# Kernel tuning notes

Hardware: AMD Instinct MI355X
Metric: run time of the kernel (lower is better)

Reference implementation:

```python
import jax, jax.numpy as jnp
import numpy as np

B, L, D, DFF, DLLM, E, TOPK = 16, 512, 768, 3072, 4096, 8, 2
EPS_GATE = 1e-9
LN_EPS = 1e-5


def _layernorm(x, gamma, beta):
    mu = jnp.mean(x, axis=-1, keepdims=True)
    var = jnp.var(x, axis=-1, keepdims=True)
    return (x - mu) * jax.lax.rsqrt(var + LN_EPS) * gamma + beta


def _mlp_block(x, w1, b1, w2, b2, gamma, beta):
    # MLPBlock: Linear -> GELU -> Linear -> LayerNorm(residual). Dropout is identity in eval.
    h = jax.nn.gelu(x @ w1 + b1)
    o = h @ w2 + b2
    return _layernorm(o + x, gamma, beta)


def setup_inputs() -> dict:
    key = jax.random.key(0)
    ks = jax.random.split(key, 24)
    sd = lambda fan_in: 1.0 / np.sqrt(fan_in)
    inp = {
        'cycle_curve_data': jax.random.normal(ks[0], (B, L, D), jnp.float32),
        'cycle_numbers': jax.random.uniform(ks[1], (B, 1), jnp.float32) * 1000.0,
        'DKP_embeddings': jax.random.normal(ks[2], (B, DLLM), jnp.float32),
        # Gate (PatternRouter_two): fuses LLM embedding + cycle number -> expert logits
        'gate_We': jax.random.normal(ks[3], (DLLM, DFF), jnp.float32) * sd(DLLM),
        'gate_Wc': jax.random.normal(ks[4], (1, DFF), jnp.float32),
        'gate_b': jnp.zeros((DFF,), jnp.float32),
        'gate_Wo': jax.random.normal(ks[5], (DFF, E), jnp.float32) * sd(DFF),
        'gate_bo': jnp.zeros((E,), jnp.float32),
        # Stacked expert params [E, ...]
        'e_w1': jax.random.normal(ks[6], (E, D, DFF), jnp.float32) * sd(D),
        'e_b1': jnp.zeros((E, DFF), jnp.float32),
        'e_w2': jax.random.normal(ks[7], (E, DFF, D), jnp.float32) * sd(DFF),
        'e_b2': jnp.zeros((E, D), jnp.float32),
        'e_gamma': jnp.ones((E, D), jnp.float32),
        'e_beta': jnp.zeros((E, D), jnp.float32),
        # General expert
        'g_w1': jax.random.normal(ks[8], (D, DFF), jnp.float32) * sd(D),
        'g_b1': jnp.zeros((DFF,), jnp.float32),
        'g_w2': jax.random.normal(ks[9], (DFF, D), jnp.float32) * sd(DFF),
        'g_b2': jnp.zeros((D,), jnp.float32),
        'g_gamma': jnp.ones((D,), jnp.float32),
        'g_beta': jnp.zeros((D,), jnp.float32),
    }
    return inp


def reference(cycle_curve_data, cycle_numbers, DKP_embeddings,
              gate_We, gate_Wc, gate_b, gate_Wo, gate_bo,
              e_w1, e_b1, e_w2, e_b2, e_gamma, e_beta,
              g_w1, g_b1, g_w2, g_b2, g_gamma, g_beta):
    # --- Router: clean logits (eval mode: no noise) ---
    h = jax.nn.relu(DKP_embeddings @ gate_We + cycle_numbers @ gate_Wc + gate_b)
    logits = h @ gate_Wo + gate_bo                         # [B, E]
    _, idx = jax.lax.top_k(logits, TOPK)                   # [B, TOPK]
    probs = jax.nn.softmax(logits, axis=1)
    mask = jnp.zeros_like(probs).at[jnp.arange(B)[:, None], idx].set(1.0)
    gated = probs * mask
    gated = gated / (jnp.sum(gated, axis=1, keepdims=True) + EPS_GATE)  # [B, E]

    # --- Experts: dense compute, zero gates zero out non-routed experts ---
    x = cycle_curve_data
    combined = jnp.zeros_like(x)
    for e in range(E):  # small fixed expert count
        out_e = _mlp_block(x, e_w1[e], e_b1[e], e_w2[e], e_b2[e], e_gamma[e], e_beta[e])
        combined = combined + gated[:, e, None, None] * out_e

    general = _mlp_block(x, g_w1, g_b1, g_w2, g_b2, g_gamma, g_beta)
    final_out = general + combined.astype(jnp.bfloat16)  # matches .to(torch.bfloat16) cast before add
    return final_out
```

## Files before the change

kernel.cpp:

```cpp
#include <hip/hip_runtime.h>
#include <cstdint>

#define B_    16
#define L_    512
#define D_    768
#define DFF_  3072
#define DLLM_ 4096
#define E_    8

typedef unsigned short ushort_t;
typedef __attribute__((ext_vector_type(4))) float accfrag_t;
typedef __attribute__((ext_vector_type(8))) short bfrag_t;

typedef __attribute__((address_space(3))) uint32_t lds_u32;
typedef __attribute__((address_space(1))) uint32_t glb_u32;

__device__ inline void gload16(const void* g, void* l) {
  __builtin_amdgcn_global_load_lds((const glb_u32*)(uintptr_t)g,
                                   (lds_u32*)(uint32_t)(uintptr_t)l, 16, 0, 0);
}

__device__ inline ushort_t f2bf(float f) {
  uint32_t u = __float_as_uint(f);
  return (ushort_t)((u + 0x7FFFu + ((u >> 16) & 1u)) >> 16);
}
__device__ inline float bf2f(ushort_t v) { return __uint_as_float(((uint32_t)v) << 16); }

#define MFMA16(a, b, c) __builtin_amdgcn_mfma_f32_16x16x32_bf16(a, b, c, 0, 0, 0)

template <int KT>
__device__ __forceinline__ void gemm_body(const char* gA, const char* gB,
                                          char* sm, accfrag_t acc[4][4]) {
  const int tid = threadIdx.x;
  const int lane = tid & 63;
  const int w = tid >> 6, wm = w >> 1, wn = w & 1;
  const int LDB = KT * 128;

  const int R0 = tid >> 3;
  const char* srcA = gA + (size_t)R0 * LDB + ((((tid & 7) ^ (R0 & 7)) << 4));
  const char* srcB = gB + (size_t)R0 * LDB + ((((tid & 7) ^ (R0 & 7)) << 4));
  const int dl = tid * 16;

  const int l15 = lane & 15, l7 = lane & 7, lhi = lane >> 4;
  const int a0 = (wm * 64 + l15) * 128 + ((lhi ^ l7) << 4);
  const int a1 = (wm * 64 + l15) * 128 + (((4 + lhi) ^ l7) << 4);
  const int b0 = 16384 + (wn * 64 + l15) * 128 + ((lhi ^ l7) << 4);
  const int b1 = 16384 + (wn * 64 + l15) * 128 + (((4 + lhi) ^ l7) << 4);

#pragma unroll 1
  for (int t = 0; t < KT; ++t) {
    const size_t ko = (size_t)t * 128;
#pragma unroll
    for (int j = 0; j < 4; ++j)
      gload16(srcA + (size_t)j * 32 * LDB + ko, sm + j * 4096 + dl);
#pragma unroll
    for (int j = 0; j < 4; ++j)
      gload16(srcB + (size_t)j * 32 * LDB + ko, sm + 16384 + j * 4096 + dl);
    __syncthreads();
    {
      bfrag_t af[4], bf[4];
#pragma unroll
      for (int nf = 0; nf < 4; ++nf) bf[nf] = *(const bfrag_t*)(sm + b0 + nf * 2048);
#pragma unroll
      for (int mf = 0; mf < 4; ++mf) af[mf] = *(const bfrag_t*)(sm + a0 + mf * 2048);
      __builtin_amdgcn_s_setprio(1);
#pragma unroll
      for (int mf = 0; mf < 4; ++mf)
#pragma unroll
        for (int nf = 0; nf < 4; ++nf)
          acc[mf][nf] = MFMA16(af[mf], bf[nf], acc[mf][nf]);
      __builtin_amdgcn_s_setprio(0);
    }
    __builtin_amdgcn_sched_barrier(0);
    {
      bfrag_t af[4], bf[4];
#pragma unroll
      for (int nf = 0; nf < 4; ++nf) bf[nf] = *(const bfrag_t*)(sm + b1 + nf * 2048);
#pragma unroll
      for (int mf = 0; mf < 4; ++mf) af[mf] = *(const bfrag_t*)(sm + a1 + mf * 2048);
      __builtin_amdgcn_s_setprio(1);
#pragma unroll
      for (int mf = 0; mf < 4; ++mf)
#pragma unroll
        for (int nf = 0; nf < 4; ++nf)
          acc[mf][nf] = MFMA16(af[mf], bf[nf], acc[mf][nf]);
      __builtin_amdgcn_s_setprio(0);
    }
    __syncthreads();
  }
}

__device__ inline void job_tile(int f, int tilesPerJob, int jp_count,
                                int& jobIdx, int& t) {
  if ((jp_count & 7) == 0) {
    const int xcd = f & 7, slot = f >> 3;
    jobIdx = xcd + 8 * (slot / tilesPerJob);
    t = slot % tilesPerJob;
  } else {
    jobIdx = f / tilesPerJob;
    t = f % tilesPerJob;
  }
}

__global__ __launch_bounds__(256, 4)
void gemm1_k(const ushort_t* __restrict__ xb, const ushort_t* __restrict__ w1t,
             const float* __restrict__ e_b1, const float* __restrict__ g_b1,
             const int* __restrict__ tidx, ushort_t* __restrict__ h_out,
             int job0, int jp_count) {
  __shared__ char sm[32768];
  int jp, t;
  job_tile(blockIdx.x, 96, jp_count, jp, t);
  const int mt = t / 24, nt = t % 24;
  const int job = job0 + jp;
  const int b = job / 3, s = job - b * 3;
  const int e = (s < 2) ? tidx[b * 2 + s] : E_;
  const char* gA = (const char*)(xb + ((size_t)b * L_ + mt * 128) * D_);
  const char* gB = (const char*)(w1t + ((size_t)e * DFF_ + nt * 128) * D_);
  accfrag_t acc[4][4] = {};
  gemm_body<12>(gA, gB, sm, acc);

  const float* b1 = (s < 2) ? (e_b1 + (size_t)e * DFF_) : g_b1;
  const int lane = threadIdx.x & 63, w = threadIdx.x >> 6;
  const int wm = w >> 1, wn = w & 1;
  const int row0 = mt * 128 + wm * 64 + ((lane >> 4) << 2);
  const int col0 = nt * 128 + wn * 64 + (lane & 15);
  float bias[4];
#pragma unroll
  for (int nf = 0; nf < 4; ++nf) bias[nf] = b1[col0 + nf * 16];
  ushort_t* hp = h_out + (size_t)jp * L_ * DFF_ + (size_t)row0 * DFF_ + col0;
#pragma unroll
  for (int mf = 0; mf < 4; ++mf)
#pragma unroll
    for (int r = 0; r < 4; ++r) {
      ushort_t* hr_ = hp + (size_t)(mf * 16 + r) * DFF_;
#pragma unroll
      for (int nf = 0; nf < 4; ++nf) {
        float v = acc[mf][nf][r] + bias[nf];
        float u = 0.7978845608028654f * (v + 0.044715f * v * v * v);
        float th = 1.0f - 2.0f / (1.0f + __expf(2.0f * u));
        hr_[nf * 16] = f2bf(0.5f * v * (1.0f + th));
      }
    }
}

__global__ __launch_bounds__(256, 4)
void gemm2_k(const ushort_t* __restrict__ h_in, const ushort_t* __restrict__ w2t,
             const float* __restrict__ e_b2, const float* __restrict__ g_b2,
             const float* __restrict__ x_f, const int* __restrict__ tidx,
             ushort_t* __restrict__ slot_o, float* __restrict__ outp,
             int job0, int jp_count) {
  __shared__ char sm[32768];
  int jp, t;
  job_tile(blockIdx.x, 24, jp_count, jp, t);
  const int mt = t / 6, nt = t % 6;
  const int job = job0 + jp;
  const int b = job / 3, s = job - b * 3;
  const int e = (s < 2) ? tidx[b * 2 + s] : E_;
  const char* gA = (const char*)(h_in + ((size_t)jp * L_ + mt * 128) * DFF_);
  const char* gB = (const char*)(w2t + ((size_t)e * D_ + nt * 128) * DFF_);
  accfrag_t acc[4][4] = {};
  gemm_body<48>(gA, gB, sm, acc);

  const float* b2 = (s < 2) ? (e_b2 + (size_t)e * D_) : g_b2;
  const int lane = threadIdx.x & 63, w = threadIdx.x >> 6;
  const int wm = w >> 1, wn = w & 1;
  const int row0 = mt * 128 + wm * 64 + ((lane >> 4) << 2);
  const int col0 = nt * 128 + wn * 64 + (lane & 15);
  float bias[4];
#pragma unroll
  for (int nf = 0; nf < 4; ++nf) bias[nf] = b2[col0 + nf * 16];
#pragma unroll
  for (int mf = 0; mf < 4; ++mf)
#pragma unroll
    for (int r = 0; r < 4; ++r) {
      const int row = row0 + mf * 16 + r;
      const float* xr = x_f + ((size_t)b * L_ + row) * D_ + col0;
#pragma unroll
      for (int nf = 0; nf < 4; ++nf) {
        float v = acc[mf][nf][r] + bias[nf] + xr[nf * 16];
        if (s < 2)
          slot_o[(((size_t)b * 2 + s) * L_ + row) * D_ + col0 + nf * 16] = f2bf(v);
        else
          outp[((size_t)b * L_ + row) * D_ + col0 + nf * 16] = v;
      }
    }
}

__global__ __launch_bounds__(256)
void transpose_cvt_k(const float* __restrict__ srcE, const float* __restrict__ srcG,
                     ushort_t* __restrict__ dst, int R, int C) {
  const int z = blockIdx.z;
  const float* src = (z < 8) ? (srcE + (size_t)z * R * C) : srcG;
  ushort_t* out = dst + (size_t)z * R * C;
  __shared__ float tile[64][65];
  const int c0 = blockIdx.x * 64, r0 = blockIdx.y * 64;
  const int t = threadIdx.x;
  const int rr = t >> 4, cc = (t & 15) * 4;
#pragma unroll
  for (int i = 0; i < 4; ++i) {
    const float4 v = *(const float4*)(src + (size_t)(r0 + rr + i * 16) * C + c0 + cc);
    tile[rr + i * 16][cc] = v.x; tile[rr + i * 16][cc + 1] = v.y;
    tile[rr + i * 16][cc + 2] = v.z; tile[rr + i * 16][cc + 3] = v.w;
  }
  __syncthreads();
  const int c = t >> 2, r8 = (t & 3) * 16;
#pragma unroll
  for (int j = 0; j < 2; ++j) {
    ushort_t u[8];
#pragma unroll
    for (int k = 0; k < 8; ++k) u[k] = f2bf(tile[r8 + j * 8 + k][c]);
    *(uint4*)(out + (size_t)(c0 + c) * R + r0 + r8 + j * 8) = *(const uint4*)u;
  }
}

__global__ void cvt_x_k(const float* __restrict__ in, ushort_t* __restrict__ out) {
  const int i = (blockIdx.x * 256 + threadIdx.x) * 4;
  const float4 v = *(const float4*)(in + i);
  uint2 u;
  u.x = (uint32_t)f2bf(v.x) | ((uint32_t)f2bf(v.y) << 16);
  u.y = (uint32_t)f2bf(v.z) | ((uint32_t)f2bf(v.w) << 16);
  *(uint2*)(out + i) = u;
}

__global__ __launch_bounds__(256)
void router_partial_k(const float* __restrict__ emb, const float* __restrict__ We,
                      float* __restrict__ rp) {
  const int nt = blockIdx.x, kb = blockIdx.y;
  const int tid = threadIdx.x;
  __shared__ float semb[B_][256];
  const int k0 = kb * 256;
#pragma unroll
  for (int r = 0; r < B_; ++r) semb[r][tid] = emb[(size_t)r * DLLM_ + k0 + tid];
  __syncthreads();
  const int f = nt * 256 + tid;
  float acc[B_] = {};
  for (int k = 0; k < 256; ++k) {
    const float wv = We[(size_t)(k0 + k) * DFF_ + f];
#pragma unroll
    for (int j = 0; j < B_; ++j) acc[j] += semb[j][k] * wv;
  }
#pragma unroll
  for (int j = 0; j < B_; ++j)
    rp[((size_t)kb * B_ + j) * DFF_ + f] = acc[j];
}

__global__ void router_reduce_k(const float* __restrict__ rp, const float* __restrict__ cyc,
                                const float* __restrict__ Wc, const float* __restrict__ gb,
                                float* __restrict__ hr) {
  const int g = blockIdx.x * 256 + threadIdx.x;
  const int b = g / DFF_, f = g - b * DFF_;
  float s = 0.0f;
#pragma unroll
  for (int kb = 0; kb < 16; ++kb)
    s += rp[((size_t)kb * B_ + b) * DFF_ + f];
  s += cyc[b] * Wc[f] + gb[f];
  hr[(size_t)b * DFF_ + f] = fmaxf(s, 0.0f);
}

__global__ void router_final_k(const float* __restrict__ hr, const float* __restrict__ Wo,
                               const float* __restrict__ bo, int* __restrict__ tidx,
                               float* __restrict__ gates) {
  const int b = blockIdx.x, tid = threadIdx.x;
  float acc[E_] = {};
  for (int f = tid; f < DFF_; f += 256) {
    const float hv = hr[(size_t)b * DFF_ + f];
#pragma unroll
    for (int o = 0; o < E_; ++o) acc[o] += hv * Wo[(size_t)f * E_ + o];
  }
  __shared__ float lred[E_][4];
#pragma unroll
  for (int o = 0; o < E_; ++o) {
    float v = acc[o];
#pragma unroll
    for (int off = 32; off > 0; off >>= 1) v += __shfl_down(v, off, 64);
    if ((tid & 63) == 0) lred[o][tid >> 6] = v;
  }
  __syncthreads();
  if (tid == 0) {
    float lg[E_];
    float mx = -1e30f;
    for (int o = 0; o < E_; ++o) {
      lg[o] = lred[o][0] + lred[o][1] + lred[o][2] + lred[o][3] + bo[o];
      mx = fmaxf(mx, lg[o]);
    }
    int i1 = 0;
    for (int o = 1; o < E_; ++o) if (lg[o] > lg[i1]) i1 = o;
    int i2 = (i1 == 0) ? 1 : 0;
    for (int o = 0; o < E_; ++o) if (o != i1 && lg[o] > lg[i2]) i2 = o;
    float p[E_], sum = 0.0f;
    for (int o = 0; o < E_; ++o) { p[o] = __expf(lg[o] - mx); sum += p[o]; }
    const float p1 = p[i1] / sum, p2 = p[i2] / sum;
    const float den = p1 + p2 + 1e-9f;
    tidx[b * 2] = i1; tidx[b * 2 + 1] = i2;
    gates[b * 2] = p1 / den; gates[b * 2 + 1] = p2 / den;
  }
}

__global__ __launch_bounds__(256)
void final_ln_k(float* __restrict__ outp, const ushort_t* __restrict__ so,
                const float* __restrict__ gates, const int* __restrict__ tidx,
                const float* __restrict__ e_gam, const float* __restrict__ e_bet,
                const float* __restrict__ g_gam, const float* __restrict__ g_bet) {
  const int row = blockIdx.x;
  const int b = row >> 9, l = row & 511;
  const int tid = threadIdx.x;
  __shared__ float red4[4];
  float* gr = outp + (size_t)row * D_;
  const ushort_t* s0 = so + (((size_t)b * 2 + 0) * L_ + l) * D_;
  const ushort_t* s1 = so + (((size_t)b * 2 + 1) * L_ + l) * D_;
  float a0[3], a1[3], a2[3];
#pragma unroll
  for (int j = 0; j < 3; ++j) {
    const int d = tid + j * 256;
    a0[j] = gr[d];
    a1[j] = bf2f(s0[d]);
    a2[j] = bf2f(s1[d]);
  }
  auto bsum = [&](float v) -> float {
#pragma unroll
    for (int o = 32; o > 0; o >>= 1) v += __shfl_down(v, o, 64);
    if ((tid & 63) == 0) red4[tid >> 6] = v;
    __syncthreads();
    const float r = red4[0] + red4[1] + red4[2] + red4[3];
    __syncthreads();
    return r;
  };
  const float sg = bsum(a0[0] + a0[1] + a0[2]);
  const float qg = bsum(a0[0] * a0[0] + a0[1] * a0[1] + a0[2] * a0[2]);
  const float s0s = bsum(a1[0] + a1[1] + a1[2]);
  const float q0s = bsum(a1[0] * a1[0] + a1[1] * a1[1] + a1[2] * a1[2]);
  const float s1s = bsum(a2[0] + a2[1] + a2[2]);
  const float q1s = bsum(a2[0] * a2[0] + a2[1] * a2[1] + a2[2] * a2[2]);
  const float inv = 1.0f / 768.0f;
  const float mug = sg * inv, rg = rsqrtf(qg * inv - mug * mug + 1e-5f);
  const float mu0 = s0s * inv, r0 = rsqrtf(q0s * inv - mu0 * mu0 + 1e-5f);
  const float mu1 = s1s * inv, r1 = rsqrtf(q1s * inv - mu1 * mu1 + 1e-5f);
  const int e0 = tidx[b * 2], e1 = tidx[b * 2 + 1];
  const float g0 = gates[b * 2], g1 = gates[b * 2 + 1];
#pragma unroll
  for (int j = 0; j < 3; ++j) {
    const int d = tid + j * 256;
    const float lng = (a0[j] - mug) * rg * g_gam[d] + g_bet[d];
    const float ln0 = (a1[j] - mu0) * r0 * e_gam[(size_t)e0 * D_ + d] + e_bet[(size_t)e0 * D_ + d];
    const float ln1 = (a2[j] - mu1) * r1 * e_gam[(size_t)e1 * D_ + d] + e_bet[(size_t)e1 * D_ + d];
    const float comb = g0 * ln0 + g1 * ln1;
    gr[d] = lng + bf2f(f2bf(comb));
  }
}

extern "C" void kernel_launch(void* const* d_in, const int* in_sizes, int n_in,
                              void* d_out, int out_size, void* d_ws, size_t ws_size,
                              hipStream_t stream) {
  const float* x_f  = (const float*)d_in[0];
  const float* cyc  = (const float*)d_in[1];
  const float* emb  = (const float*)d_in[2];
  const float* We   = (const float*)d_in[3];
  const float* Wc   = (const float*)d_in[4];
  const float* gb   = (const float*)d_in[5];
  const float* Wo   = (const float*)d_in[6];
  const float* bo   = (const float*)d_in[7];
  const float* e_w1 = (const float*)d_in[8];
  const float* e_b1 = (const float*)d_in[9];
  const float* e_w2 = (const float*)d_in[10];
  const float* e_b2 = (const float*)d_in[11];
  const float* e_gam = (const float*)d_in[12];
  const float* e_bet = (const float*)d_in[13];
  const float* g_w1 = (const float*)d_in[14];
  const float* g_b1 = (const float*)d_in[15];
  const float* g_w2 = (const float*)d_in[16];
  const float* g_b2 = (const float*)d_in[17];
  const float* g_gam = (const float*)d_in[18];
  const float* g_bet = (const float*)d_in[19];
  float* outp = (float*)d_out;
  char* ws = (char*)d_ws;

  size_t off = 0;
  auto alloc = [&](size_t bytes) { size_t o = off; off = (off + bytes + 255) & ~(size_t)255; return o; };
  const size_t o_idx  = alloc(32 * 4);
  const size_t o_gate = alloc(32 * 4);
  const size_t o_hr   = alloc((size_t)B_ * DFF_ * 4);
  const size_t o_rp   = alloc((size_t)16 * B_ * DFF_ * 4);
  const size_t o_xb   = alloc((size_t)B_ * L_ * D_ * 2);
  const size_t o_w1t  = alloc((size_t)9 * DFF_ * D_ * 2);
  const size_t o_w2t  = alloc((size_t)9 * D_ * DFF_ * 2);
  const size_t o_so   = alloc((size_t)B_ * 2 * L_ * D_ * 2);
  const size_t o_h    = off;

  int JP = 1;
  const int divs[10] = {48, 24, 16, 12, 8, 6, 4, 3, 2, 1};
  for (int k = 0; k < 10; ++k) {
    if (o_h + (size_t)divs[k] * L_ * DFF_ * 2 <= ws_size) { JP = divs[k]; break; }
  }

  ushort_t* xb    = (ushort_t*)(ws + o_xb);
  ushort_t* w1t   = (ushort_t*)(ws + o_w1t);
  ushort_t* w2t   = (ushort_t*)(ws + o_w2t);
  ushort_t* so    = (ushort_t*)(ws + o_so);
  ushort_t* h_ws  = (ushort_t*)(ws + o_h);
  int*      tidx  = (int*)(ws + o_idx);
  float*    gates = (float*)(ws + o_gate);
  float*    hr    = (float*)(ws + o_hr);
  float*    rp    = (float*)(ws + o_rp);

  cvt_x_k<<<dim3((B_ * L_ * D_) / 1024), dim3(256), 0, stream>>>(x_f, xb);
  transpose_cvt_k<<<dim3(DFF_ / 64, D_ / 64, 9), dim3(256), 0, stream>>>(e_w1, g_w1, w1t, D_, DFF_);
  transpose_cvt_k<<<dim3(D_ / 64, DFF_ / 64, 9), dim3(256), 0, stream>>>(e_w2, g_w2, w2t, DFF_, D_);
  router_partial_k<<<dim3(12, 16), dim3(256), 0, stream>>>(emb, We, rp);
  router_reduce_k<<<dim3(192), dim3(256), 0, stream>>>(rp, cyc, Wc, gb, hr);
  router_final_k<<<dim3(16), dim3(256), 0, stream>>>(hr, Wo, bo, tidx, gates);

  const int passes = 48 / JP;
  for (int p = 0; p < passes; ++p) {
    gemm1_k<<<dim3(96 * JP), dim3(256), 0, stream>>>(xb, w1t, e_b1, g_b1, tidx, h_ws, p * JP, JP);
    gemm2_k<<<dim3(24 * JP), dim3(256), 0, stream>>>(h_ws, w2t, e_b2, g_b2, x_f, tidx, so, outp, p * JP, JP);
  }
  final_ln_k<<<dim3(B_ * L_), dim3(256), 0, stream>>>(outp, so, gates, tidx,
                                                      e_gam, e_bet, g_gam, g_bet);
}
```

Baseline: 477.8 us.

## Widen GEMM tiles to 128x192 and fuse router reduce into final router kernel

Both expert GEMMs now use 128x192 output tiles, so each wave holds a 4x6 grid of MFMA accumulators. LDS grows to 40KB and launch bounds drop to 3 blocks per CU. The wider tile raises arithmetic intensity per shared-memory load, at the cost of more registers, lower occupancy and fewer blocks per pass. Separately, the router reduce kernel is folded into router_final_k, which removes one launch and the intermediate hr buffer, though the reduction now runs on only 16 blocks.

Result: faster. 437.3 us (median of 2 runs) (-8.5%).

```diff
diff --git a/kernel.cpp b/kernel.cpp
--- a/kernel.cpp
+++ b/kernel.cpp
@@ -30,22 +30,23 @@
 
 template <int KT>
 __device__ __forceinline__ void gemm_body(const char* gA, const char* gB,
-                                          char* sm, accfrag_t acc[4][4]) {
+                                          char* sm, accfrag_t acc[4][6]) {
   const int tid = threadIdx.x;
   const int lane = tid & 63;
   const int w = tid >> 6, wm = w >> 1, wn = w & 1;
   const int LDB = KT * 128;
 
   const int R0 = tid >> 3;
-  const char* srcA = gA + (size_t)R0 * LDB + ((((tid & 7) ^ (R0 & 7)) << 4));
-  const char* srcB = gB + (size_t)R0 * LDB + ((((tid & 7) ^ (R0 & 7)) << 4));
+  const int swz = (((tid & 7) ^ (R0 & 7)) << 4);
+  const char* srcA = gA + (size_t)R0 * LDB + swz;
+  const char* srcB = gB + (size_t)R0 * LDB + swz;
   const int dl = tid * 16;
 
   const int l15 = lane & 15, l7 = lane & 7, lhi = lane >> 4;
   const int a0 = (wm * 64 + l15) * 128 + ((lhi ^ l7) << 4);
   const int a1 = (wm * 64 + l15) * 128 + (((4 + lhi) ^ l7) << 4);
-  const int b0 = 16384 + (wn * 64 + l15) * 128 + ((lhi ^ l7) << 4);
-  const int b1 = 16384 + (wn * 64 + l15) * 128 + (((4 + lhi) ^ l7) << 4);
+  const int b0 = 16384 + (wn * 96 + l15) * 128 + ((lhi ^ l7) << 4);
+  const int b1 = 16384 + (wn * 96 + l15) * 128 + (((4 + lhi) ^ l7) << 4);
 
 #pragma unroll 1
   for (int t = 0; t < KT; ++t) {
@@ -54,35 +55,35 @@
     for (int j = 0; j < 4; ++j)
       gload16(srcA + (size_t)j * 32 * LDB + ko, sm + j * 4096 + dl);
 #pragma unroll
-    for (int j = 0; j < 4; ++j)
+    for (int j = 0; j < 6; ++j)
       gload16(srcB + (size_t)j * 32 * LDB + ko, sm + 16384 + j * 4096 + dl);
     __syncthreads();
     {
-      bfrag_t af[4], bf[4];
-#pragma unroll
-      for (int nf = 0; nf < 4; ++nf) bf[nf] = *(const bfrag_t*)(sm + b0 + nf * 2048);
+      bfrag_t af[4], bf[6];
+#pragma unroll
+      for (int nf = 0; nf < 6; ++nf) bf[nf] = *(const bfrag_t*)(sm + b0 + nf * 2048);
 #pragma unroll
       for (int mf = 0; mf < 4; ++mf) af[mf] = *(const bfrag_t*)(sm + a0 + mf * 2048);
       __builtin_amdgcn_s_setprio(1);
 #pragma unroll
       for (int mf = 0; mf < 4; ++mf)
 #pragma unroll
-        for (int nf = 0; nf < 4; ++nf)
+        for (int nf = 0; nf < 6; ++nf)
           acc[mf][nf] = MFMA16(af[mf], bf[nf], acc[mf][nf]);
       __builtin_amdgcn_s_setprio(0);
     }
     __builtin_amdgcn_sched_barrier(0);
     {
-      bfrag_t af[4], bf[4];
-#pragma unroll
-      for (int nf = 0; nf < 4; ++nf) bf[nf] = *(const bfrag_t*)(sm + b1 + nf * 2048);
+      bfrag_t af[4], bf[6];
+#pragma unroll
+      for (int nf = 0; nf < 6; ++nf) bf[nf] = *(const bfrag_t*)(sm + b1 + nf * 2048);
 #pragma unroll
       for (int mf = 0; mf < 4; ++mf) af[mf] = *(const bfrag_t*)(sm + a1 + mf * 2048);
       __builtin_amdgcn_s_setprio(1);
 #pragma unroll
       for (int mf = 0; mf < 4; ++mf)
 #pragma unroll
-        for (int nf = 0; nf < 4; ++nf)
+        for (int nf = 0; nf < 6; ++nf)
           acc[mf][nf] = MFMA16(af[mf], bf[nf], acc[mf][nf]);
       __builtin_amdgcn_s_setprio(0);
     }
@@ -102,31 +103,31 @@
   }
 }
 
-__global__ __launch_bounds__(256, 4)
+__global__ __launch_bounds__(256, 3)
 void gemm1_k(const ushort_t* __restrict__ xb, const ushort_t* __restrict__ w1t,
              const float* __restrict__ e_b1, const float* __restrict__ g_b1,
              const int* __restrict__ tidx, ushort_t* __restrict__ h_out,
              int job0, int jp_count) {
-  __shared__ char sm[32768];
+  __shared__ char sm[40960];
   int jp, t;
-  job_tile(blockIdx.x, 96, jp_count, jp, t);
-  const int mt = t / 24, nt = t % 24;
+  job_tile(blockIdx.x, 64, jp_count, jp, t);
+  const int mt = t >> 4, nt = t & 15;
   const int job = job0 + jp;
   const int b = job / 3, s = job - b * 3;
   const int e = (s < 2) ? tidx[b * 2 + s] : E_;
   const char* gA = (const char*)(xb + ((size_t)b * L_ + mt * 128) * D_);
-  const char* gB = (const char*)(w1t + ((size_t)e * DFF_ + nt * 128) * D_);
-  accfrag_t acc[4][4] = {};
+  const char* gB = (const char*)(w1t + ((size_t)e * DFF_ + nt * 192) * D_);
+  accfrag_t acc[4][6] = {};
   gemm_body<12>(gA, gB, sm, acc);
 
   const float* b1 = (s < 2) ? (e_b1 + (size_t)e * DFF_) : g_b1;
   const int lane = threadIdx.x & 63, w = threadIdx.x >> 6;
   const int wm = w >> 1, wn = w & 1;
   const int row0 = mt * 128 + wm * 64 + ((lane >> 4) << 2);
-  const int col0 = nt * 128 + wn * 64 + (lane & 15);
-  float bias[4];
-#pragma unroll
-  for (int nf = 0; nf < 4; ++nf) bias[nf] = b1[col0 + nf * 16];
+  const int col0 = nt * 192 + wn * 96 + (lane & 15);
+  float bias[6];
+#pragma unroll
+  for (int nf = 0; nf < 6; ++nf) bias[nf] = b1[col0 + nf * 16];
   ushort_t* hp = h_out + (size_t)jp * L_ * DFF_ + (size_t)row0 * DFF_ + col0;
 #pragma unroll
   for (int mf = 0; mf < 4; ++mf)
@@ -134,7 +135,7 @@
     for (int r = 0; r < 4; ++r) {
       ushort_t* hr_ = hp + (size_t)(mf * 16 + r) * DFF_;
 #pragma unroll
-      for (int nf = 0; nf < 4; ++nf) {
+      for (int nf = 0; nf < 6; ++nf) {
         float v = acc[mf][nf][r] + bias[nf];
         float u = 0.7978845608028654f * (v + 0.044715f * v * v * v);
         float th = 1.0f - 2.0f / (1.0f + __expf(2.0f * u));
@@ -143,32 +144,32 @@
     }
 }
 
-__global__ __launch_bounds__(256, 4)
+__global__ __launch_bounds__(256, 3)
 void gemm2_k(const ushort_t* __restrict__ h_in, const ushort_t* __restrict__ w2t,
              const float* __restrict__ e_b2, const float* __restrict__ g_b2,
              const float* __restrict__ x_f, const int* __restrict__ tidx,
              ushort_t* __restrict__ slot_o, float* __restrict__ outp,
              int job0, int jp_count) {
-  __shared__ char sm[32768];
+  __shared__ char sm[40960];
   int jp, t;
-  job_tile(blockIdx.x, 24, jp_count, jp, t);
-  const int mt = t / 6, nt = t % 6;
+  job_tile(blockIdx.x, 16, jp_count, jp, t);
+  const int mt = t >> 2, nt = t & 3;
   const int job = job0 + jp;
   const int b = job / 3, s = job - b * 3;
   const int e = (s < 2) ? tidx[b * 2 + s] : E_;
   const char* gA = (const char*)(h_in + ((size_t)jp * L_ + mt * 128) * DFF_);
-  const char* gB = (const char*)(w2t + ((size_t)e * D_ + nt * 128) * DFF_);
-  accfrag_t acc[4][4] = {};
+  const char* gB = (const char*)(w2t + ((size_t)e * D_ + nt * 192) * DFF_);
+  accfrag_t acc[4][6] = {};
   gemm_body<48>(gA, gB, sm, acc);
 
   const float* b2 = (s < 2) ? (e_b2 + (size_t)e * D_) : g_b2;
   const int lane = threadIdx.x & 63, w = threadIdx.x >> 6;
   const int wm = w >> 1, wn = w & 1;
   const int row0 = mt * 128 + wm * 64 + ((lane >> 4) << 2);
-  const int col0 = nt * 128 + wn * 64 + (lane & 15);
-  float bias[4];
-#pragma unroll
-  for (int nf = 0; nf < 4; ++nf) bias[nf] = b2[col0 + nf * 16];
+  const int col0 = nt * 192 + wn * 96 + (lane & 15);
+  float bias[6];
+#pragma unroll
+  for (int nf = 0; nf < 6; ++nf) bias[nf] = b2[col0 + nf * 16];
 #pragma unroll
   for (int mf = 0; mf < 4; ++mf)
 #pragma unroll
@@ -176,7 +177,7 @@
       const int row = row0 + mf * 16 + r;
       const float* xr = x_f + ((size_t)b * L_ + row) * D_ + col0;
 #pragma unroll
-      for (int nf = 0; nf < 4; ++nf) {
+      for (int nf = 0; nf < 6; ++nf) {
         float v = acc[mf][nf][r] + bias[nf] + xr[nf * 16];
         if (s < 2)
           slot_o[(((size_t)b * 2 + s) * L_ + row) * D_ + col0 + nf * 16] = f2bf(v);
@@ -244,28 +245,25 @@
     rp[((size_t)kb * B_ + j) * DFF_ + f] = acc[j];
 }
 
-__global__ void router_reduce_k(const float* __restrict__ rp, const float* __restrict__ cyc,
-                                const float* __restrict__ Wc, const float* __restrict__ gb,
-                                float* __restrict__ hr) {
-  const int g = blockIdx.x * 256 + threadIdx.x;
-  const int b = g / DFF_, f = g - b * DFF_;
-  float s = 0.0f;
-#pragma unroll
-  for (int kb = 0; kb < 16; ++kb)
-    s += rp[((size_t)kb * B_ + b) * DFF_ + f];
-  s += cyc[b] * Wc[f] + gb[f];
-  hr[(size_t)b * DFF_ + f] = fmaxf(s, 0.0f);
-}
-
-__global__ void router_final_k(const float* __restrict__ hr, const float* __restrict__ Wo,
-                               const float* __restrict__ bo, int* __restrict__ tidx,
-                               float* __restrict__ gates) {
+__global__ __launch_bounds__(256)
+void router_final_k(const float* __restrict__ rp, const float* __restrict__ cyc,
+                    const float* __restrict__ Wc, const float* __restrict__ gb,
+                    const float* __restrict__ Wo, const float* __restrict__ bo,
+                    int* __restrict__ tidx, float* __restrict__ gates) {
   const int b = blockIdx.x, tid = threadIdx.x;
+  const float cycb = cyc[b];
   float acc[E_] = {};
-  for (int f = tid; f < DFF_; f += 256) {
-    const float hv = hr[(size_t)b * DFF_ + f];
-#pragma unroll
-    for (int o = 0; o < E_; ++o) acc[o] += hv * Wo[(size_t)f * E_ + o];
+#pragma unroll
+  for (int fi = 0; fi < 12; ++fi) {
+    const int f = tid + fi * 256;
+    float sv = 0.0f;
+#pragma unroll
+    for (int kb = 0; kb < 16; ++kb)
+      sv += rp[((size_t)kb * B_ + b) * DFF_ + f];
+    sv += cycb * Wc[f] + gb[f];
+    sv = fmaxf(sv, 0.0f);
+#pragma unroll
+    for (int o = 0; o < E_; ++o) acc[o] += sv * Wo[(size_t)f * E_ + o];
   }
   __shared__ float lred[E_][4];
 #pragma unroll
@@ -378,7 +376,6 @@
   auto alloc = [&](size_t bytes) { size_t o = off; off = (off + bytes + 255) & ~(size_t)255; return o; };
   const size_t o_idx  = alloc(32 * 4);
   const size_t o_gate = alloc(32 * 4);
-  const size_t o_hr   = alloc((size_t)B_ * DFF_ * 4);
   const size_t o_rp   = alloc((size_t)16 * B_ * DFF_ * 4);
   const size_t o_xb   = alloc((size_t)B_ * L_ * D_ * 2);
   const size_t o_w1t  = alloc((size_t)9 * DFF_ * D_ * 2);
@@ -399,20 +396,18 @@
   ushort_t* h_ws  = (ushort_t*)(ws + o_h);
   int*      tidx  = (int*)(ws + o_idx);
   float*    gates = (float*)(ws + o_gate);
-  float*    hr    = (float*)(ws + o_hr);
   float*    rp    = (float*)(ws + o_rp);
 
   cvt_x_k<<<dim3((B_ * L_ * D_) / 1024), dim3(256), 0, stream>>>(x_f, xb);
   transpose_cvt_k<<<dim3(DFF_ / 64, D_ / 64, 9), dim3(256), 0, stream>>>(e_w1, g_w1, w1t, D_, DFF_);
   transpose_cvt_k<<<dim3(D_ / 64, DFF_ / 64, 9), dim3(256), 0, stream>>>(e_w2, g_w2, w2t, DFF_, D_);
   router_partial_k<<<dim3(12, 16), dim3(256), 0, stream>>>(emb, We, rp);
-  router_reduce_k<<<dim3(192), dim3(256), 0, stream>>>(rp, cyc, Wc, gb, hr);
-  router_final_k<<<dim3(16), dim3(256), 0, stream>>>(hr, Wo, bo, tidx, gates);
+  router_final_k<<<dim3(16), dim3(256), 0, stream>>>(rp, cyc, Wc, gb, Wo, bo, tidx, gates);
 
   const int passes = 48 / JP;
   for (int p = 0; p < passes; ++p) {
-    gemm1_k<<<dim3(96 * JP), dim3(256), 0, stream>>>(xb, w1t, e_b1, g_b1, tidx, h_ws, p * JP, JP);
-    gemm2_k<<<dim3(24 * JP), dim3(256), 0, stream>>>(h_ws, w2t, e_b2, g_b2, x_f, tidx, so, outp, p * JP, JP);
+    gemm1_k<<<dim3(64 * JP), dim3(256), 0, stream>>>(xb, w1t, e_b1, g_b1, tidx, h_ws, p * JP, JP);
+    gemm2_k<<<dim3(16 * JP), dim3(256), 0, stream>>>(h_ws, w2t, e_b2, g_b2, x_f, tidx, so, outp, p * JP, JP);
   }
   final_ln_k<<<dim3(B_ * L_), dim3(256), 0, stream>>>(outp, so, gates, tidx,
                                                       e_gam, e_bet, g_gam, g_bet);
```
